# Kernel optimization log

Hardware: AMD Instinct MI355X
Metric: run time of the kernel (lower is better)

## Reference

```python
import jax, jax.numpy as jnp
import numpy as np
from jax import lax

B, C, H, W = 8, 256, 64, 64
E, K, OUT = 9, 3, 256
EPS = 1e-5


def setup_inputs() -> dict:
    key = jax.random.key(0)
    ks = jax.random.split(key, 12)
    return {
        "x": jax.random.normal(ks[0], (B, C, H, W), jnp.float32),
        "w_experts": jax.random.normal(ks[1], (E, C, K, K), jnp.float32) * 0.1,  # depthwise kernels (O=C, I=1 folded)
        "bn_gamma": jax.random.normal(ks[2], (E, C), jnp.float32) * 0.1 + 1.0,
        "bn_beta": jax.random.normal(ks[3], (E, C), jnp.float32) * 0.1,
        "bn_mean": jax.random.normal(ks[4], (E, C), jnp.float32) * 0.1,
        "bn_var": jax.random.uniform(ks[5], (E, C), jnp.float32, 0.5, 1.5),
        "scales": jnp.full((E, C), 0.1, jnp.float32),
        "w_out": jax.random.normal(ks[6], (OUT, C), jnp.float32) * (1.0 / np.sqrt(C)),  # 1x1 conv weight
        "out_gamma": jax.random.normal(ks[7], (OUT,), jnp.float32) * 0.1 + 1.0,
        "out_beta": jax.random.normal(ks[8], (OUT,), jnp.float32) * 0.1,
        "out_mean": jax.random.normal(ks[9], (OUT,), jnp.float32) * 0.1,
        "out_var": jax.random.uniform(ks[10], (OUT,), jnp.float32, 0.5, 1.5),
    }


def reference(x, w_experts, bn_gamma, bn_beta, bn_mean, bn_var, scales,
              w_out, out_gamma, out_beta, out_mean, out_var):
    # All E depthwise convs in ONE grouped conv: groups=C, E outputs per group.
    # kernel (E,C,K,K) -> (C,E,K,K) -> (C*E, 1, K, K); output group c holds experts of channel c.
    k = jnp.transpose(w_experts, (1, 0, 2, 3)).reshape(C * E, 1, K, K)
    y = lax.conv_general_dilated(
        x, k, window_strides=(1, 1), padding="SAME",
        feature_group_count=C,
        dimension_numbers=("NCHW", "OIHW", "NCHW"),
    )  # [B, C*E, H, W]
    y = y.reshape(x.shape[0], C, E, H, W)

    # Fold BN (eval-mode, running stats) and per-expert channel scale, then sum over experts.
    t = bn_gamma * lax.rsqrt(bn_var + EPS)          # [E, C]
    eff_scale = t * scales                          # [E, C]
    eff_bias = ((bn_beta - bn_mean * t) * scales).sum(0)  # [C]
    moe = jnp.einsum("bcehw,ec->bchw", y, eff_scale) + eff_bias[None, :, None, None]
    moe = jax.nn.silu(moe)

    # out_prj: 1x1 conv + BN + SiLU
    out = jnp.einsum("bchw,oc->bohw", moe, w_out)
    t2 = out_gamma * lax.rsqrt(out_var + EPS)       # [OUT]
    out = out * t2[None, :, None, None] + (out_beta - out_mean * t2)[None, :, None, None]
    return jax.nn.silu(out)
```

## Files before the change

kernel.cpp:

```cpp
#include <hip/hip_runtime.h>

#define EPS 1e-5f

typedef __attribute__((ext_vector_type(8))) __bf16 bf16x8;
typedef __attribute__((ext_vector_type(4))) float f32x4;

__device__ __forceinline__ float silu_f(float v) {
  return v / (1.f + __expf(-v));
}

__global__ __launch_bounds__(256) void prep_kernel(
    const float* __restrict__ w_experts, const float* __restrict__ bn_gamma,
    const float* __restrict__ bn_beta, const float* __restrict__ bn_mean,
    const float* __restrict__ bn_var, const float* __restrict__ scales,
    const float* __restrict__ w_out, const float* __restrict__ out_gamma,
    const float* __restrict__ out_beta, const float* __restrict__ out_mean,
    const float* __restrict__ out_var,
    float* __restrict__ eff_kernel, __bf16* __restrict__ w_eff,
    float* __restrict__ bias2)
{
  const int t = threadIdx.x;
  if (blockIdx.x == 0) {
    const int c = t;
    float k9[9];
#pragma unroll
    for (int r = 0; r < 9; ++r) k9[r] = 0.f;
    float bias = 0.f;
    for (int e = 0; e < 9; ++e) {
      const int ec = e * 256 + c;
      const float tt = bn_gamma[ec] * rsqrtf(bn_var[ec] + EPS);
      const float sc = scales[ec];
      const float es = tt * sc;
      bias += (bn_beta[ec] - bn_mean[ec] * tt) * sc;
      const float* wp = w_experts + (size_t)ec * 9;
#pragma unroll
      for (int r = 0; r < 9; ++r) k9[r] += es * wp[r];
    }
#pragma unroll
    for (int r = 0; r < 9; ++r) eff_kernel[c * 12 + r] = k9[r];
    eff_kernel[c * 12 + 9]  = bias;
    eff_kernel[c * 12 + 10] = 0.f;
    eff_kernel[c * 12 + 11] = 0.f;
    const float t2 = out_gamma[c] * rsqrtf(out_var[c] + EPS);
    bias2[c] = out_beta[c] - out_mean[c] * t2;
  } else {
    const int i = (blockIdx.x - 1) * 256 + t;
    const int o = i >> 8;
    const float t2 = out_gamma[o] * rsqrtf(out_var[o] + EPS);
    w_eff[i] = (__bf16)(w_out[i] * t2);
  }
}

__global__ __launch_bounds__(1024, 4) void fused_kernel(
    const float* __restrict__ x, const float* __restrict__ eff_kernel,
    const __bf16* __restrict__ w_eff, const float* __restrict__ bias2,
    float* __restrict__ out)
{
  __shared__ __align__(16) __bf16 B_lds[128 * 264];
  __shared__ __align__(16) float kern_s[256 * 12];

  const int t = threadIdx.x;
  const int id = blockIdx.x;
  const int b = id & 7;
  const int h0 = (id >> 3) * 2;

  for (int i = t; i < 3072; i += 1024) kern_s[i] = eff_kernel[i];

  const int lane = t & 63;
  const int wv = t >> 6;
  const int lg = lane >> 4;
  const int wq = lane & 15;
  const int w4 = wq * 4;
  const bool up_ok = (h0 > 0), dn_ok = (h0 < 62);
  const float4 z4 = make_float4(0.f, 0.f, 0.f, 0.f);

  auto dw_loads = [&](int it, float4* v) {
    const int ch = it * 64 + wv * 4 + lg;
    const float* xc = x + (size_t)(b * 256 + ch) * 4096 + w4;
    v[1] = *(const float4*)(xc + h0 * 64);
    v[2] = *(const float4*)(xc + (h0 + 1) * 64);
    v[0] = up_ok ? *(const float4*)(xc + (h0 - 1) * 64) : z4;
    v[3] = dn_ok ? *(const float4*)(xc + (h0 + 2) * 64) : z4;
  };

  auto dw_compute = [&](int it, const float4* v) {
    const int ch = it * 64 + wv * 4 + lg;
    const f32x4* kp = (const f32x4*)(kern_s + ch * 12);
    const f32x4 ka = kp[0], kb = kp[1], kc = kp[2];
    float rowv[4][6];
#pragma unroll
    for (int r = 0; r < 4; ++r) {
      const float vl = __shfl_up(v[r].w, 1);
      const float vr = __shfl_down(v[r].x, 1);
      rowv[r][0] = (wq == 0) ? 0.f : vl;
      rowv[r][1] = v[r].x; rowv[r][2] = v[r].y;
      rowv[r][3] = v[r].z; rowv[r][4] = v[r].w;
      rowv[r][5] = (wq == 15) ? 0.f : vr;
    }
    const float k0 = ka[0], k1 = ka[1], k2 = ka[2];
    const float k3 = ka[3], k4 = kb[0], k5 = kb[1];
    const float k6 = kb[2], k7 = kb[3], k8 = kc[0];
    const float bias = kc[1];
#pragma unroll
    for (int rr = 0; rr < 2; ++rr) {
#pragma unroll
      for (int j = 0; j < 4; ++j) {
        float s = bias
          + k0 * rowv[rr][j]     + k1 * rowv[rr][j + 1]     + k2 * rowv[rr][j + 2]
          + k3 * rowv[rr + 1][j] + k4 * rowv[rr + 1][j + 1] + k5 * rowv[rr + 1][j + 2]
          + k6 * rowv[rr + 2][j] + k7 * rowv[rr + 2][j + 1] + k8 * rowv[rr + 2][j + 2];
        B_lds[(rr * 64 + w4 + j) * 264 + ch] = (__bf16)silu_f(s);
      }
    }
  };

  const int wrow   = wv >> 3;
  const int wave_o = (wv & 7) * 32;
  const int quad = lg, l15 = wq;

  f32x4 acc[2][4];
#pragma unroll
  for (int i = 0; i < 2; ++i)
#pragma unroll
    for (int j = 0; j < 4; ++j) acc[i][j] = (f32x4){0.f, 0.f, 0.f, 0.f};

  auto gemm_step = [&](int kk) {
    bf16x8 af[2], bv[4];
#pragma unroll
    for (int i = 0; i < 2; ++i)
      af[i] = *(const bf16x8*)&w_eff[(size_t)(wave_o + i * 16 + l15) * 256 + kk * 32 + quad * 8];
#pragma unroll
    for (int j = 0; j < 4; ++j)
      bv[j] = *(const bf16x8*)&B_lds[(wrow * 64 + j * 16 + l15) * 264 + kk * 32 + quad * 8];
#pragma unroll
    for (int i = 0; i < 2; ++i)
#pragma unroll
      for (int j = 0; j < 4; ++j)
        acc[i][j] = __builtin_amdgcn_mfma_f32_16x16x32_bf16(af[i], bv[j], acc[i][j], 0, 0, 0);
  };

  float4 va[4], vb[4];
  dw_loads(0, va); dw_loads(1, vb);
  __syncthreads();
  dw_compute(0, va); dw_compute(1, vb);
  __syncthreads();
  dw_loads(2, va);
  gemm_step(0); gemm_step(1);
  dw_compute(2, va);
  dw_loads(3, vb);
  gemm_step(2); gemm_step(3);
  dw_compute(3, vb);
  __syncthreads();
  gemm_step(4); gemm_step(5); gemm_step(6); gemm_step(7);

  float* outb = out + (size_t)(b * 256) * 4096 + (size_t)(h0 + wrow) * 64;
#pragma unroll
  for (int i = 0; i < 2; ++i) {
#pragma unroll
    for (int r = 0; r < 4; ++r) {
      const int o = wave_o + i * 16 + quad * 4 + r;
      const float bo = bias2[o];
#pragma unroll
      for (int j = 0; j < 4; ++j) {
        const int p = j * 16 + l15;
        outb[(size_t)o * 4096 + p] = silu_f(acc[i][j][r] + bo);
      }
    }
  }
}

extern "C" void kernel_launch(void* const* d_in, const int* in_sizes, int n_in,
                              void* d_out, int out_size, void* d_ws, size_t ws_size,
                              hipStream_t stream) {
  const float* x         = (const float*)d_in[0];
  const float* w_experts = (const float*)d_in[1];
  const float* bn_gamma  = (const float*)d_in[2];
  const float* bn_beta   = (const float*)d_in[3];
  const float* bn_mean   = (const float*)d_in[4];
  const float* bn_var    = (const float*)d_in[5];
  const float* scales    = (const float*)d_in[6];
  const float* w_out     = (const float*)d_in[7];
  const float* out_gamma = (const float*)d_in[8];
  const float* out_beta  = (const float*)d_in[9];
  const float* out_mean  = (const float*)d_in[10];
  const float* out_var   = (const float*)d_in[11];
  float* out = (float*)d_out;

  char* ws = (char*)d_ws;
  float* eff_kernel = (float*)(ws);
  __bf16* w_eff     = (__bf16*)(ws + 12288);
  float* bias2      = (float*)(ws + 143360);

  hipLaunchKernelGGL(prep_kernel, dim3(257), dim3(256), 0, stream,
                     w_experts, bn_gamma, bn_beta, bn_mean, bn_var, scales,
                     w_out, out_gamma, out_beta, out_mean, out_var,
                     eff_kernel, w_eff, bias2);
  hipLaunchKernelGGL(fused_kernel, dim3(256), dim3(1024), 0, stream,
                     x, eff_kernel, w_eff, bias2, out);
}
```

Baseline: 127.0 us.

## Process one image row per block with 512 threads and swizzled LDS layout

Each block now handles a single output row (512 blocks of 512 threads) instead of two rows with 1024 threads, halving the LDS B tile. The depthwise and GEMM stages are re-pipelined in finer chunks, an XOR swizzle is applied to LDS writes and reads to cut bank conflicts, and MFMA sections get raised wave priority. The aim is more blocks and better overlap per CU. The cost is that halo rows are reloaded across more blocks (3 row loads per output row instead of 2), raising global read traffic, and each block also reloads the kernel and weights.

Result: slower. 130.0 us (+2.4%).

```diff
diff --git a/kernel.cpp b/kernel.cpp
--- a/kernel.cpp
+++ b/kernel.cpp
@@ -51,45 +51,42 @@
   }
 }
 
-__global__ __launch_bounds__(1024, 4) void fused_kernel(
+__global__ __launch_bounds__(512, 4) void fused_kernel(
     const float* __restrict__ x, const float* __restrict__ eff_kernel,
     const __bf16* __restrict__ w_eff, const float* __restrict__ bias2,
     float* __restrict__ out)
 {
-  __shared__ __align__(16) __bf16 B_lds[128 * 264];
+  __shared__ __align__(16) __bf16 B_lds[64 * 264];
   __shared__ __align__(16) float kern_s[256 * 12];
 
   const int t = threadIdx.x;
   const int id = blockIdx.x;
   const int b = id & 7;
-  const int h0 = (id >> 3) * 2;
-
-  for (int i = t; i < 3072; i += 1024) kern_s[i] = eff_kernel[i];
+  const int h = id >> 3;
 
   const int lane = t & 63;
   const int wv = t >> 6;
   const int lg = lane >> 4;
   const int wq = lane & 15;
   const int w4 = wq * 4;
-  const bool up_ok = (h0 > 0), dn_ok = (h0 < 62);
+  const bool up_ok = (h > 0), dn_ok = (h < 63);
   const float4 z4 = make_float4(0.f, 0.f, 0.f, 0.f);
 
   auto dw_loads = [&](int it, float4* v) {
-    const int ch = it * 64 + wv * 4 + lg;
+    const int ch = it * 32 + wv * 4 + lg;
     const float* xc = x + (size_t)(b * 256 + ch) * 4096 + w4;
-    v[1] = *(const float4*)(xc + h0 * 64);
-    v[2] = *(const float4*)(xc + (h0 + 1) * 64);
-    v[0] = up_ok ? *(const float4*)(xc + (h0 - 1) * 64) : z4;
-    v[3] = dn_ok ? *(const float4*)(xc + (h0 + 2) * 64) : z4;
+    v[1] = *(const float4*)(xc + h * 64);
+    v[0] = up_ok ? *(const float4*)(xc + (h - 1) * 64) : z4;
+    v[2] = dn_ok ? *(const float4*)(xc + (h + 1) * 64) : z4;
   };
 
   auto dw_compute = [&](int it, const float4* v) {
-    const int ch = it * 64 + wv * 4 + lg;
+    const int ch = it * 32 + wv * 4 + lg;
     const f32x4* kp = (const f32x4*)(kern_s + ch * 12);
     const f32x4 ka = kp[0], kb = kp[1], kc = kp[2];
-    float rowv[4][6];
-#pragma unroll
-    for (int r = 0; r < 4; ++r) {
+    float rowv[3][6];
+#pragma unroll
+    for (int r = 0; r < 3; ++r) {
       const float vl = __shfl_up(v[r].w, 1);
       const float vr = __shfl_down(v[r].x, 1);
       rowv[r][0] = (wq == 0) ? 0.f : vl;
@@ -97,26 +94,18 @@
       rowv[r][3] = v[r].z; rowv[r][4] = v[r].w;
       rowv[r][5] = (wq == 15) ? 0.f : vr;
     }
-    const float k0 = ka[0], k1 = ka[1], k2 = ka[2];
-    const float k3 = ka[3], k4 = kb[0], k5 = kb[1];
-    const float k6 = kb[2], k7 = kb[3], k8 = kc[0];
-    const float bias = kc[1];
-#pragma unroll
-    for (int rr = 0; rr < 2; ++rr) {
-#pragma unroll
-      for (int j = 0; j < 4; ++j) {
-        float s = bias
-          + k0 * rowv[rr][j]     + k1 * rowv[rr][j + 1]     + k2 * rowv[rr][j + 2]
-          + k3 * rowv[rr + 1][j] + k4 * rowv[rr + 1][j + 1] + k5 * rowv[rr + 1][j + 2]
-          + k6 * rowv[rr + 2][j] + k7 * rowv[rr + 2][j + 1] + k8 * rowv[rr + 2][j + 2];
-        B_lds[(rr * 64 + w4 + j) * 264 + ch] = (__bf16)silu_f(s);
-      }
+    const int swzc = ((ch >> 3) ^ (wq & 7)) * 8 + (ch & 7);
+#pragma unroll
+    for (int j = 0; j < 4; ++j) {
+      float s = kc[1]
+        + ka[0] * rowv[0][j] + ka[1] * rowv[0][j + 1] + ka[2] * rowv[0][j + 2]
+        + ka[3] * rowv[1][j] + kb[0] * rowv[1][j + 1] + kb[1] * rowv[1][j + 2]
+        + kb[2] * rowv[2][j] + kb[3] * rowv[2][j + 1] + kc[0] * rowv[2][j + 2];
+      B_lds[(w4 + j) * 264 + swzc] = (__bf16)silu_f(s);
     }
   };
 
-  const int wrow   = wv >> 3;
-  const int wave_o = (wv & 7) * 32;
-  const int quad = lg, l15 = wq;
+  const int wave_o = wv * 32;
 
   f32x4 acc[2][4];
 #pragma unroll
@@ -128,41 +117,52 @@
     bf16x8 af[2], bv[4];
 #pragma unroll
     for (int i = 0; i < 2; ++i)
-      af[i] = *(const bf16x8*)&w_eff[(size_t)(wave_o + i * 16 + l15) * 256 + kk * 32 + quad * 8];
-#pragma unroll
-    for (int j = 0; j < 4; ++j)
-      bv[j] = *(const bf16x8*)&B_lds[(wrow * 64 + j * 16 + l15) * 264 + kk * 32 + quad * 8];
+      af[i] = *(const bf16x8*)&w_eff[(size_t)(wave_o + i * 16 + wq) * 256 + kk * 32 + lg * 8];
+#pragma unroll
+    for (int j = 0; j < 4; ++j) {
+      const int p = j * 16 + wq;
+      const int swz = (kk * 4 + lg) ^ ((p >> 2) & 7);
+      bv[j] = *(const bf16x8*)&B_lds[p * 264 + swz * 8];
+    }
+    __builtin_amdgcn_s_setprio(1);
 #pragma unroll
     for (int i = 0; i < 2; ++i)
 #pragma unroll
       for (int j = 0; j < 4; ++j)
         acc[i][j] = __builtin_amdgcn_mfma_f32_16x16x32_bf16(af[i], bv[j], acc[i][j], 0, 0, 0);
+    __builtin_amdgcn_s_setprio(0);
   };
 
-  float4 va[4], vb[4];
+  float4 va[3], vb[3];
   dw_loads(0, va); dw_loads(1, vb);
+  for (int i = t; i < 3072; i += 512) kern_s[i] = eff_kernel[i];
   __syncthreads();
-  dw_compute(0, va); dw_compute(1, vb);
+  dw_compute(0, va); dw_loads(2, va);
+  dw_compute(1, vb); dw_loads(3, vb);
+  dw_compute(2, va); dw_compute(3, vb);
   __syncthreads();
-  dw_loads(2, va);
-  gemm_step(0); gemm_step(1);
-  dw_compute(2, va);
-  dw_loads(3, vb);
-  gemm_step(2); gemm_step(3);
-  dw_compute(3, vb);
+  dw_loads(4, va);
+  gemm_step(0);
+  dw_compute(4, va); dw_loads(5, vb);
+  gemm_step(1);
+  dw_compute(5, vb); dw_loads(6, va);
+  gemm_step(2);
+  dw_compute(6, va); dw_loads(7, vb);
+  gemm_step(3);
+  dw_compute(7, vb);
   __syncthreads();
   gemm_step(4); gemm_step(5); gemm_step(6); gemm_step(7);
 
-  float* outb = out + (size_t)(b * 256) * 4096 + (size_t)(h0 + wrow) * 64;
+  float* outb = out + (size_t)(b * 256) * 4096 + (size_t)h * 64;
 #pragma unroll
   for (int i = 0; i < 2; ++i) {
 #pragma unroll
     for (int r = 0; r < 4; ++r) {
-      const int o = wave_o + i * 16 + quad * 4 + r;
+      const int o = wave_o + i * 16 + lg * 4 + r;
       const float bo = bias2[o];
 #pragma unroll
       for (int j = 0; j < 4; ++j) {
-        const int p = j * 16 + l15;
+        const int p = j * 16 + wq;
         outb[(size_t)o * 4096 + p] = silu_f(acc[i][j][r] + bo);
       }
     }
@@ -195,6 +195,6 @@
                      w_experts, bn_gamma, bn_beta, bn_mean, bn_var, scales,
                      w_out, out_gamma, out_beta, out_mean, out_var,
                      eff_kernel, w_eff, bias2);
-  hipLaunchKernelGGL(fused_kernel, dim3(256), dim3(1024), 0, stream,
+  hipLaunchKernelGGL(fused_kernel, dim3(512), dim3(512), 0, stream,
                      x, eff_kernel, w_eff, bias2, out);
 }
```
